# Optimization experiments

Measured on AMD Instinct MI355X. Metric: run time of the kernel, lower is better.

Reference implementation:

```python
import jax, jax.numpy as jnp
import numpy as np

N = 50000      # nodes
H = 128        # hidden_size
RBF = 20       # edge_embedding_size
E_CHE = 400000 # chemical edges
E_VDW = 200000 # van-der-Waals edges


def _prelu(x, a):
    return jnp.where(x > 0, x, a * x)


def _mlp(x, w1, b1, a1, w2, b2, a2):
    # Linear -> PReLU -> Linear -> PReLU (PaiNN message / filter MLP)
    h = _prelu(x @ w1 + b1, a1)
    return _prelu(h @ w2 + b2, a2)


def setup_inputs() -> dict:
    key = jax.random.key(0)
    ks = list(jax.random.split(key, 64))
    it = iter(ks)
    d = {}
    d['node_scalar'] = jax.random.normal(next(it), (N, H), jnp.float32)
    d['node_vector'] = jax.random.normal(next(it), (N, 3, H), jnp.float32)
    for pfx, E in (('che', E_CHE), ('vdw', E_VDW)):
        d[pfx + '_edge'] = jax.random.randint(next(it), (E, 2), 0, N)
        d[pfx + '_edge_diff'] = jax.random.normal(next(it), (E, 3), jnp.float32)
        d[pfx + '_edge_dist'] = jax.random.uniform(next(it), (E,), jnp.float32) + 0.5  # strictly positive
        d[pfx + '_rbf_dist'] = jax.random.normal(next(it), (E, RBF), jnp.float32)
    # four 2-layer MLPs with per-layer PReLU scalar slope (torch default init 0.25)
    def mlp_params(pfx, din):
        s1 = 1.0 / np.sqrt(din)
        s2 = 1.0 / np.sqrt(H)
        d[pfx + '_w1'] = jax.random.uniform(next(it), (din, H), jnp.float32, -s1, s1)
        d[pfx + '_b1'] = jax.random.uniform(next(it), (H,), jnp.float32, -s1, s1)
        d[pfx + '_a1'] = jnp.asarray(0.25, jnp.float32)
        d[pfx + '_w2'] = jax.random.uniform(next(it), (H, 3 * H), jnp.float32, -s2, s2)
        d[pfx + '_b2'] = jax.random.uniform(next(it), (3 * H,), jnp.float32, -s2, s2)
        d[pfx + '_a2'] = jnp.asarray(0.25, jnp.float32)
    mlp_params('che_s', H)    # che scalar message MLP
    mlp_params('che_f', RBF)  # che filter layer
    mlp_params('vdw_s', H)
    mlp_params('vdw_f', RBF)
    return d


def _branch(node_scalar, node_vector, edge, edge_diff, edge_dist, rbf, sp, fp):
    # sp/fp: 6-tuples of MLP params. edge[:,1]=source gather, edge[:,0]=dest scatter.
    scalar_out = _mlp(node_scalar, *sp)          # [N, 3H]
    filter_w = _mlp(rbf, *fp)                    # [E, 3H]
    filter_out = scalar_out[edge[:, 1]] * filter_w  # gather + gate
    gate_vector, message_scalar, gate_edge = jnp.split(filter_out, 3, axis=1)
    state_vector = node_vector[edge[:, 1]] * gate_vector[:, None, :]        # [E,3,H]
    unit = edge_diff / edge_dist[:, None]                                    # [E,3]
    edge_vector = unit[:, :, None] * gate_edge[:, None, :]                   # [E,3,H]
    message_vector = state_vector + edge_vector
    res_scalar = jax.ops.segment_sum(message_scalar, edge[:, 0], num_segments=N)
    res_vector = jax.ops.segment_sum(message_vector, edge[:, 0], num_segments=N)
    return res_scalar, res_vector


def reference(node_scalar, node_vector,
              che_edge, che_edge_diff, che_edge_dist, che_rbf_dist,
              vdw_edge, vdw_edge_diff, vdw_edge_dist, vdw_rbf_dist,
              che_s_w1, che_s_b1, che_s_a1, che_s_w2, che_s_b2, che_s_a2,
              che_f_w1, che_f_b1, che_f_a1, che_f_w2, che_f_b2, che_f_a2,
              vdw_s_w1, vdw_s_b1, vdw_s_a1, vdw_s_w2, vdw_s_b2, vdw_s_a2,
              vdw_f_w1, vdw_f_b1, vdw_f_a1, vdw_f_w2, vdw_f_b2, vdw_f_a2):
    che_sp = (che_s_w1, che_s_b1, che_s_a1, che_s_w2, che_s_b2, che_s_a2)
    che_fp = (che_f_w1, che_f_b1, che_f_a1, che_f_w2, che_f_b2, che_f_a2)
    vdw_sp = (vdw_s_w1, vdw_s_b1, vdw_s_a1, vdw_s_w2, vdw_s_b2, vdw_s_a2)
    vdw_fp = (vdw_f_w1, vdw_f_b1, vdw_f_a1, vdw_f_w2, vdw_f_b2, vdw_f_a2)
    che_rs, che_rv = _branch(node_scalar, node_vector, che_edge, che_edge_diff,
                             che_edge_dist, che_rbf_dist, che_sp, che_fp)
    vdw_rs, vdw_rv = _branch(node_scalar, node_vector, vdw_edge, vdw_edge_diff,
                             vdw_edge_dist, vdw_rbf_dist, vdw_sp, vdw_fp)
    return (node_scalar + che_rs + vdw_rs, node_vector + che_rv + vdw_rv)
```

## Files before the change

### kernel.cpp

```cpp
#include <hip/hip_runtime.h>
#include <hip/hip_bf16.h>

typedef float f32x4 __attribute__((ext_vector_type(4)));
typedef short bf16x8 __attribute__((ext_vector_type(8)));

#define HD 128
#define SCAN_TILE 2048

__device__ __forceinline__ float prelu_f(float x, float a) {
  return x > 0.f ? x : a * x;
}

__device__ __forceinline__ unsigned short f2bf(float x) {
  __hip_bfloat16 h = __float2bfloat16(x);
  return *reinterpret_cast<unsigned short*>(&h);
}
__device__ __forceinline__ float bf2f(unsigned short u) {
  union { unsigned u; float f; } a; a.u = ((unsigned)u) << 16;
  return a.f;
}
__device__ __forceinline__ f32x4 bf4_to_f32(ushort4 u) {
  f32x4 r; r[0] = bf2f(u.x); r[1] = bf2f(u.y); r[2] = bf2f(u.z); r[3] = bf2f(u.w);
  return r;
}

__global__ __launch_bounds__(256) void init_out_kernel(
    const f32x4* __restrict__ ns, const f32x4* __restrict__ nv,
    f32x4* __restrict__ out, int n_ns4, int n_nv4)
{
  int total = n_ns4 + n_nv4;
  for (int i = blockIdx.x * 256 + threadIdx.x; i < total; i += gridDim.x * 256)
    out[i] = (i < n_ns4) ? ns[i] : nv[i - n_ns4];
}

__global__ __launch_bounds__(256) void tconv_kernel(
    const float* __restrict__ src, unsigned short* __restrict__ dst)
{
  int idx = blockIdx.x * 256 + threadIdx.x;
  if (idx < 384 * 128) {
    int c = idx >> 7, k = idx & 127;
    dst[idx] = f2bf(src[(size_t)k * 384 + c]);
  }
}

__global__ __launch_bounds__(256) void tconv_w1e_kernel(
    const float* __restrict__ src, unsigned short* __restrict__ dst)
{
  int idx = blockIdx.x * 256 + threadIdx.x;
  if (idx < 128 * 32) {
    int c = idx >> 5, k = idx & 31;
    dst[idx] = (k < 20) ? f2bf(src[(size_t)k * 128 + c]) : (unsigned short)0;
  }
}

__global__ __launch_bounds__(256) void tconv_w1n_kernel(
    const float* __restrict__ src, unsigned short* __restrict__ dst)
{
  int idx = blockIdx.x * 256 + threadIdx.x;
  if (idx < 128 * 128) {
    int c = idx >> 7, k = idx & 127;
    dst[idx] = f2bf(src[(size_t)k * 128 + c]);
  }
}

__global__ __launch_bounds__(256) void conv_bf16_kernel(
    const f32x4* __restrict__ src, ushort4* __restrict__ dst, int n4)
{
  int i = blockIdx.x * 256 + threadIdx.x;
  if (i < n4) {
    f32x4 v = src[i];
    ushort4 o;
    o.x = f2bf(v[0]); o.y = f2bf(v[1]); o.z = f2bf(v[2]); o.w = f2bf(v[3]);
    dst[i] = o;
  }
}

__global__ __launch_bounds__(256) void node_mlp_mfma(
    const unsigned short* __restrict__ Abf,
    const unsigned short* __restrict__ w1t,
    const float* __restrict__ b1, const float* __restrict__ a1p,
    const unsigned short* __restrict__ w2t,
    const float* __restrict__ b2, const float* __restrict__ a2p,
    unsigned short* __restrict__ out,
    int M)
{
  __shared__ __attribute__((aligned(16))) unsigned short A_lds[64 * HD];
  __shared__ __attribute__((aligned(16))) unsigned short h_lds[64 * HD];
  const int t = threadIdx.x;
  const int wvid = t >> 6, lane = t & 63, l15 = lane & 15, l4 = lane >> 4;
  const int m0 = blockIdx.x * 64;
  const float a1 = a1p[0], a2 = a2p[0];

  for (int idx = t; idx < 64 * HD / 8; idx += 256) {
    int row = idx >> 4, seg = (idx & 15) * 8;
    bf16x8 v = 0;
    if (m0 + row < M) v = *(const bf16x8*)&Abf[(size_t)(m0 + row) * HD + seg];
    *(bf16x8*)&A_lds[row * HD + (seg ^ ((row & 7) << 3))] = v;
  }
  __syncthreads();

  {
    bf16x8 Bf[2][4];
    #pragma unroll
    for (int nf = 0; nf < 2; nf++)
      #pragma unroll
      for (int ks = 0; ks < 4; ks++) {
        int col = wvid * 32 + nf * 16 + l15;
        Bf[nf][ks] = *(const bf16x8*)&w1t[(size_t)col * 128 + ks * 32 + l4 * 8];
      }
    f32x4 D[4][2];
    #pragma unroll
    for (int mi = 0; mi < 4; mi++)
      #pragma unroll
      for (int nf = 0; nf < 2; nf++)
        #pragma unroll
        for (int cc = 0; cc < 4; cc++) D[mi][nf][cc] = 0.f;

    #pragma unroll
    for (int mi = 0; mi < 4; mi++)
      #pragma unroll
      for (int ks = 0; ks < 4; ks++) {
        int row = mi * 16 + l15;
        bf16x8 Af = *(const bf16x8*)&A_lds[row * HD + ((ks * 32 + l4 * 8) ^ ((row & 7) << 3))];
        D[mi][0] = __builtin_amdgcn_mfma_f32_16x16x32_bf16(Af, Bf[0][ks], D[mi][0], 0, 0, 0);
        D[mi][1] = __builtin_amdgcn_mfma_f32_16x16x32_bf16(Af, Bf[1][ks], D[mi][1], 0, 0, 0);
      }

    float b1v0 = b1[wvid * 32 + l15];
    float b1v1 = b1[wvid * 32 + 16 + l15];
    #pragma unroll
    for (int mi = 0; mi < 4; mi++)
      #pragma unroll
      for (int nf = 0; nf < 2; nf++)
        #pragma unroll
        for (int r4 = 0; r4 < 4; r4++) {
          int row = mi * 16 + l4 * 4 + r4;
          int col = wvid * 32 + nf * 16 + l15;
          h_lds[row * HD + (col ^ ((row & 7) << 3))] =
              f2bf(prelu_f(D[mi][nf][r4] + (nf ? b1v1 : b1v0), a1));
        }
  }
  __syncthreads();

  for (int m = 0; m < 3; m++) {
    bf16x8 Bf[2][4];
    #pragma unroll
    for (int nf = 0; nf < 2; nf++)
      #pragma unroll
      for (int ks = 0; ks < 4; ks++) {
        int col = m * 128 + wvid * 32 + nf * 16 + l15;
        Bf[nf][ks] = *(const bf16x8*)&w2t[(size_t)col * 128 + ks * 32 + l4 * 8];
      }
    f32x4 D[4][2];
    #pragma unroll
    for (int mi = 0; mi < 4; mi++)
      #pragma unroll
      for (int nf = 0; nf < 2; nf++)
        #pragma unroll
        for (int cc = 0; cc < 4; cc++) D[mi][nf][cc] = 0.f;

    #pragma unroll
    for (int mi = 0; mi < 4; mi++)
      #pragma unroll
      for (int ks = 0; ks < 4; ks++) {
        int row = mi * 16 + l15;
        bf16x8 Af = *(const bf16x8*)&h_lds[row * HD + ((ks * 32 + l4 * 8) ^ ((row & 7) << 3))];
        D[mi][0] = __builtin_amdgcn_mfma_f32_16x16x32_bf16(Af, Bf[0][ks], D[mi][0], 0, 0, 0);
        D[mi][1] = __builtin_amdgcn_mfma_f32_16x16x32_bf16(Af, Bf[1][ks], D[mi][1], 0, 0, 0);
      }

    float b2v0 = b2[m * 128 + wvid * 32 + l15];
    float b2v1 = b2[m * 128 + wvid * 32 + 16 + l15];
    #pragma unroll
    for (int mi = 0; mi < 4; mi++)
      #pragma unroll
      for (int nf = 0; nf < 2; nf++)
        #pragma unroll
        for (int r4 = 0; r4 < 4; r4++) {
          int row = mi * 16 + l4 * 4 + r4;
          if (m0 + row < M) {
            int col = m * 128 + wvid * 32 + nf * 16 + l15;
            out[(size_t)(m0 + row) * 384 + col] =
                f2bf(prelu_f(D[mi][nf][r4] + (nf ? b2v1 : b2v0), a2));
          }
        }
  }
}

__global__ __launch_bounds__(256) void zero_int_kernel(int* __restrict__ p, int n) {
  int i = blockIdx.x * 256 + threadIdx.x;
  if (i < n) p[i] = 0;
}

__global__ __launch_bounds__(256) void hist_kernel(const int* __restrict__ edge, int* __restrict__ counts, int E) {
  int e = blockIdx.x * 256 + threadIdx.x;
  if (e < E) atomicAdd(&counts[edge[(size_t)e * 2]], 1);
}

__global__ __launch_bounds__(256) void scan_partial_kernel(
    const int* __restrict__ counts, int* __restrict__ partials, int n)
{
  const int b = blockIdx.x, t = threadIdx.x;
  const int base = b * SCAN_TILE + t * 8;
  int s = 0;
  #pragma unroll
  for (int i = 0; i < 8; i++) {
    int idx = base + i;
    if (idx < n) s += counts[idx];
  }
  __shared__ int sums[256];
  sums[t] = s;
  __syncthreads();
  for (int o = 128; o > 0; o >>= 1) {
    if (t < o) sums[t] += sums[t + o];
    __syncthreads();
  }
  if (t == 0) partials[b] = sums[0];
}

__global__ __launch_bounds__(256) void scan_partials_kernel(int* __restrict__ partials, int nb)
{
  __shared__ int s[256];
  const int t = threadIdx.x;
  s[t] = (t < nb) ? partials[t] : 0;
  __syncthreads();
  for (int o = 1; o < 256; o <<= 1) {
    int v = s[t];
    int u = (t >= o) ? s[t - o] : 0;
    __syncthreads();
    s[t] = v + u;
    __syncthreads();
  }
  if (t < nb) partials[t] = (t == 0) ? 0 : s[t - 1];
}

__global__ __launch_bounds__(256) void scan_write_kernel(
    const int* __restrict__ counts, const int* __restrict__ partials,
    int* __restrict__ offsets, int* __restrict__ cursor, int n, int E)
{
  const int b = blockIdx.x, t = threadIdx.x;
  const int base = b * SCAN_TILE + t * 8;
  int vals[8];
  int s = 0;
  #pragma unroll
  for (int i = 0; i < 8; i++) {
    int idx = base + i;
    vals[i] = (idx < n) ? counts[idx] : 0;
    s += vals[i];
  }
  __shared__ int sums[256];
  sums[t] = s;
  __syncthreads();
  for (int o = 1; o < 256; o <<= 1) {
    int v = sums[t];
    int u = (t >= o) ? sums[t - o] : 0;
    __syncthreads();
    sums[t] = v + u;
    __syncthreads();
  }
  int run = partials[b] + ((t == 0) ? 0 : sums[t - 1]);
  #pragma unroll
  for (int i = 0; i < 8; i++) {
    int idx = base + i;
    if (idx < n) {
      offsets[idx] = run;
      cursor[idx] = run;
      run += vals[i];
    }
  }
  if (b == 0 && t == 0) offsets[n] = E;
}

__global__ __launch_bounds__(256) void scatter_ids_kernel(
    const int* __restrict__ edge, int* __restrict__ cursor, int* __restrict__ edge_list, int E)
{
  int e = blockIdx.x * 256 + threadIdx.x;
  if (e < E) {
    int d = edge[(size_t)e * 2];
    int p = atomicAdd(&cursor[d], 1);
    edge_list[p] = e;
  }
}

__global__ __launch_bounds__(256) void permute_edge_kernel(
    const int* __restrict__ edge_list,
    const int* __restrict__ edge, const float* __restrict__ diff,
    const float* __restrict__ dist, const float* __restrict__ rbf,
    int* __restrict__ src_s, int* __restrict__ dst_s,
    float4* __restrict__ unit_s, unsigned short* __restrict__ rbf_b,
    int E)
{
  int p = blockIdx.x * 256 + threadIdx.x;
  if (p >= E) return;
  int e = edge_list[p];
  src_s[p] = edge[(size_t)e * 2 + 1];
  dst_s[p] = edge[(size_t)e * 2 + 0];
  float inv = 1.f / dist[e];
  float4 u;
  u.x = diff[(size_t)e * 3 + 0] * inv;
  u.y = diff[(size_t)e * 3 + 1] * inv;
  u.z = diff[(size_t)e * 3 + 2] * inv;
  u.w = 0.f;
  unit_s[p] = u;
  ushort4* ro = (ushort4*)(rbf_b + (size_t)p * 32);
  const float* rr = &rbf[(size_t)e * 20];
  #pragma unroll
  for (int i = 0; i < 5; i++) {
    ushort4 o;
    o.x = f2bf(rr[4 * i + 0]); o.y = f2bf(rr[4 * i + 1]);
    o.z = f2bf(rr[4 * i + 2]); o.w = f2bf(rr[4 * i + 3]);
    ro[i] = o;
  }
  ushort4 z; z.x = 0; z.y = 0; z.z = 0; z.w = 0;
  ro[5] = z; ro[6] = z; ro[7] = z;
}

__global__ __launch_bounds__(256) void edge_mfma_reduce_kernel(
    const unsigned short* __restrict__ so,
    const unsigned short* __restrict__ nv,
    const int*   __restrict__ src_s,
    const int*   __restrict__ dst_s,
    const float4* __restrict__ unit_s,
    const unsigned short* __restrict__ rbf_b,
    const int*   __restrict__ offsets,
    const unsigned short* __restrict__ w1t,
    const float* __restrict__ b1, const float* __restrict__ a1p,
    const unsigned short* __restrict__ w2t,
    const float* __restrict__ b2, const float* __restrict__ a2p,
    float* __restrict__ out,
    int N, int E)
{
  __shared__ __attribute__((aligned(16))) unsigned short A1_lds[64 * 40];
  __shared__ __attribute__((aligned(16))) unsigned short h_lds[64 * HD];
  __shared__ __attribute__((aligned(16))) unsigned short P_lds[3][64 * HD];
  __shared__ int src_l[64];
  __shared__ float unit_l[64][3];
  __shared__ int run_rs[65], run_node[64], run_flag[64];
  __shared__ int nd_s;

  const int t = threadIdx.x;
  const int tx = t & 31, ty = t >> 5;
  const int c4 = tx * 4;
  const int wvid = t >> 6, lane = t & 63, l15 = lane & 15, l4 = lane >> 4;
  const int pblk = blockIdx.x * 64;
  const int nrows = min(64, E - pblk);
  const float a1 = a1p[0], a2 = a2p[0];

  if (t < 64) {
    int d = -1, s = 0;
    float ux = 0.f, uy = 0.f, uz = 0.f;
    if (t < nrows) {
      s = src_s[pblk + t];
      d = dst_s[pblk + t];
      float4 u = unit_s[pblk + t];
      ux = u.x; uy = u.y; uz = u.z;
    }
    src_l[t] = s;
    unit_l[t][0] = ux; unit_l[t][1] = uy; unit_l[t][2] = uz;
    int dprev = __shfl_up(d, 1);
    bool flag = (t < nrows) && (t == 0 || d != dprev);
    unsigned long long mask = __ballot(flag ? 1 : 0);
    if (flag) {
      int j = __popcll(mask & ((1ull << t) - 1ull));
      run_rs[j] = t;
      run_node[j] = d;
      unsigned long long rest = (t == 63) ? 0ull : (mask >> (t + 1));
      int re = rest ? (t + 1 + (__ffsll((long long)rest) - 1)) : nrows;
      int interior = 1;
      if (t == 0 && offsets[d] != pblk) interior = 0;
      if (re == nrows && offsets[d + 1] != pblk + nrows) interior = 0;
      run_flag[j] = interior;
    }
    if (t == 0) {
      int nd = __popcll(mask);
      nd_s = nd;
      run_rs[nd] = nrows;
    }
  }

  {
    const bf16x8* rb = (const bf16x8*)(rbf_b + (size_t)pblk * 32);
    int row = t >> 2, seg = (t & 3) * 8;
    *(bf16x8*)&A1_lds[row * 40 + seg] = rb[t];
  }
  __syncthreads();

  {
    bf16x8 B1[2];
    B1[0] = *(const bf16x8*)&w1t[(size_t)(wvid * 32 + l15) * 32 + l4 * 8];
    B1[1] = *(const bf16x8*)&w1t[(size_t)(wvid * 32 + 16 + l15) * 32 + l4 * 8];
    f32x4 D1[4][2];
    #pragma unroll
    for (int mi = 0; mi < 4; mi++)
      #pragma unroll
      for (int nf = 0; nf < 2; nf++)
        #pragma unroll
        for (int cc = 0; cc < 4; cc++) D1[mi][nf][cc] = 0.f;

    #pragma unroll
    for (int mi = 0; mi < 4; mi++) {
      bf16x8 Af = *(const bf16x8*)&A1_lds[(mi * 16 + l15) * 40 + l4 * 8];
      D1[mi][0] = __builtin_amdgcn_mfma_f32_16x16x32_bf16(Af, B1[0], D1[mi][0], 0, 0, 0);
      D1[mi][1] = __builtin_amdgcn_mfma_f32_16x16x32_bf16(Af, B1[1], D1[mi][1], 0, 0, 0);
    }

    float b1v0 = b1[wvid * 32 + l15];
    float b1v1 = b1[wvid * 32 + 16 + l15];
    #pragma unroll
    for (int mi = 0; mi < 4; mi++)
      #pragma unroll
      for (int nf = 0; nf < 2; nf++)
        #pragma unroll
        for (int r4 = 0; r4 < 4; r4++) {
          int row = mi * 16 + l4 * 4 + r4;
          int col = wvid * 32 + nf * 16 + l15;
          h_lds[row * HD + (col ^ ((row & 7) << 3))] =
              f2bf(prelu_f(D1[mi][nf][r4] + (nf ? b1v1 : b1v0), a1));
        }
  }
  __syncthreads();

  for (int m = 0; m < 3; m++) {
    bf16x8 Bf[2][4];
    #pragma unroll
    for (int nf = 0; nf < 2; nf++)
      #pragma unroll
      for (int ks = 0; ks < 4; ks++) {
        int col = m * 128 + wvid * 32 + nf * 16 + l15;
        Bf[nf][ks] = *(const bf16x8*)&w2t[(size_t)col * 128 + ks * 32 + l4 * 8];
      }
    f32x4 D[4][2];
    #pragma unroll
    for (int mi = 0; mi < 4; mi++)
      #pragma unroll
      for (int nf = 0; nf < 2; nf++)
        #pragma unroll
        for (int cc = 0; cc < 4; cc++) D[mi][nf][cc] = 0.f;

    #pragma unroll
    for (int mi = 0; mi < 4; mi++)
      #pragma unroll
      for (int ks = 0; ks < 4; ks++) {
        int row = mi * 16 + l15;
        bf16x8 Af = *(const bf16x8*)&h_lds[row * HD + ((ks * 32 + l4 * 8) ^ ((row & 7) << 3))];
        D[mi][0] = __builtin_amdgcn_mfma_f32_16x16x32_bf16(Af, Bf[0][ks], D[mi][0], 0, 0, 0);
        D[mi][1] = __builtin_amdgcn_mfma_f32_16x16x32_bf16(Af, Bf[1][ks], D[mi][1], 0, 0, 0);
      }

    float b2v0 = b2[m * 128 + wvid * 32 + l15];
    float b2v1 = b2[m * 128 + wvid * 32 + 16 + l15];
    #pragma unroll
    for (int mi = 0; mi < 4; mi++)
      #pragma unroll
      for (int nf = 0; nf < 2; nf++)
        #pragma unroll
        for (int r4 = 0; r4 < 4; r4++) {
          int row = mi * 16 + l4 * 4 + r4;
          int col = wvid * 32 + nf * 16 + l15;
          float v = prelu_f(D[mi][nf][r4] + (nf ? b2v1 : b2v0), a2);
          P_lds[m][row * HD + (col ^ ((row & 7) << 3))] = f2bf(v);
        }
  }
  __syncthreads();

  #pragma unroll
  for (int rr = 0; rr < 8; rr++) {
    const int r = ty * 8 + rr;
    const int src = src_l[r];
    const int sc = c4 ^ ((r & 7) << 3);
    f32x4 gvp = bf4_to_f32(*(const ushort4*)&P_lds[0][r * HD + sc]);
    f32x4 msp = bf4_to_f32(*(const ushort4*)&P_lds[1][r * HD + sc]);
    f32x4 gep = bf4_to_f32(*(const ushort4*)&P_lds[2][r * HD + sc]);
    const size_t sb = (size_t)src * 384;
    f32x4 s0 = bf4_to_f32(*(const ushort4*)&so[sb + c4]);
    f32x4 s1 = bf4_to_f32(*(const ushort4*)&so[sb + HD + c4]);
    f32x4 s2 = bf4_to_f32(*(const ushort4*)&so[sb + 2 * HD + c4]);
    f32x4 v0 = bf4_to_f32(*(const ushort4*)&nv[sb + c4]);
    f32x4 v1 = bf4_to_f32(*(const ushort4*)&nv[sb + HD + c4]);
    f32x4 v2 = bf4_to_f32(*(const ushort4*)&nv[sb + 2 * HD + c4]);
    const float u0 = unit_l[r][0], u1 = unit_l[r][1], u2 = unit_l[r][2];
    ushort4 msw, m0w, m1w, m2w;
    #pragma unroll
    for (int cc = 0; cc < 4; cc++) {
      float gv = gvp[cc] * s0[cc];
      float ms = msp[cc] * s1[cc];
      float ge = gep[cc] * s2[cc];
      float mv0 = v0[cc] * gv + u0 * ge;
      float mv1 = v1[cc] * gv + u1 * ge;
      float mv2 = v2[cc] * gv + u2 * ge;
      ((unsigned short*)&msw)[cc] = f2bf(ms);
      ((unsigned short*)&m0w)[cc] = f2bf(mv0);
      ((unsigned short*)&m1w)[cc] = f2bf(mv1);
      ((unsigned short*)&m2w)[cc] = f2bf(mv2);
    }
    *(ushort4*)&h_lds[r * HD + sc]    = msw;
    *(ushort4*)&P_lds[0][r * HD + sc] = m0w;
    *(ushort4*)&P_lds[1][r * HD + sc] = m1w;
    *(ushort4*)&P_lds[2][r * HD + sc] = m2w;
  }
  __syncthreads();

  {
    const int pl = t >> 6;
    const int c2 = (t & 63) * 2;
    const unsigned short* region = (pl == 0) ? h_lds : &P_lds[pl - 1][0];
    float* out_v = out + (size_t)N * HD;
    const int nd = nd_s;
    for (int j = 0; j < nd; j++) {
      const int rs = run_rs[j], re = run_rs[j + 1];
      const int n = run_node[j];
      float a0 = 0.f, a1v = 0.f;
      for (int r = rs; r < re; r++) {
        int ad = r * HD + (((c2 & ~3) ^ ((r & 7) << 3)) | (c2 & 3));
        unsigned int u = *(const unsigned int*)&region[ad];
        a0  += bf2f((unsigned short)(u & 0xffffu));
        a1v += bf2f((unsigned short)(u >> 16));
      }
      float* dstp = (pl == 0) ? (out + (size_t)n * HD + c2)
                              : (out_v + (size_t)n * 384 + (size_t)(pl - 1) * HD + c2);
      if (run_flag[j]) {
        float2 cur = *(float2*)dstp;
        cur.x += a0; cur.y += a1v;
        *(float2*)dstp = cur;
      } else {
        atomicAdd(dstp, a0);
        atomicAdd(dstp + 1, a1v);
      }
    }
  }
}

extern "C" void kernel_launch(void* const* d_in, const int* in_sizes, int n_in,
                              void* d_out, int out_size, void* d_ws, size_t ws_size,
                              hipStream_t stream)
{
  const float* node_scalar = (const float*)d_in[0];
  const float* node_vector = (const float*)d_in[1];
  const int*   che_edge = (const int*)d_in[2];
  const float* che_diff = (const float*)d_in[3];
  const float* che_dist = (const float*)d_in[4];
  const float* che_rbf  = (const float*)d_in[5];
  const int*   vdw_edge = (const int*)d_in[6];
  const float* vdw_diff = (const float*)d_in[7];
  const float* vdw_dist = (const float*)d_in[8];
  const float* vdw_rbf  = (const float*)d_in[9];
  const float* mlp_p[24];
  for (int i = 0; i < 24; i++) mlp_p[i] = (const float*)d_in[10 + i];

  const int N = in_sizes[0] / HD;
  const int E_che = in_sizes[4];
  const int E_vdw = in_sizes[8];
  const int E_max = E_che > E_vdw ? E_che : E_vdw;
  const int E_pad = (E_max + 63) & ~63;
  const int nb_scan = (N + SCAN_TILE - 1) / SCAN_TILE;

  char* wp = (char*)d_ws;
  size_t off = 0;
  unsigned short* so_bf = (unsigned short*)(wp + off); off += (size_t)N * 384 * 2;
  unsigned short* nv_bf = (unsigned short*)(wp + off); off += (size_t)N * 384 * 2;
  unsigned short* ns_bf = (unsigned short*)(wp + off); off += (size_t)N * 128 * 2;
  int* counts     = (int*)(wp + off);   off += (size_t)N * 4;
  int* cursor     = (int*)(wp + off);   off += (size_t)N * 4;
  int* offsets    = (int*)(wp + off);   off += (size_t)(N + 1) * 4;
  int* partials   = (int*)(wp + off);   off += 256 * 4;
  off = (off + 255) & ~(size_t)255;
  int* edge_list  = (int*)(wp + off);   off += (size_t)E_max * 4;
  int* src_s      = (int*)(wp + off);   off += (size_t)E_max * 4;
  int* dst_s      = (int*)(wp + off);   off += (size_t)E_max * 4;
  off = (off + 255) & ~(size_t)255;
  float4* unit_s  = (float4*)(wp + off); off += (size_t)E_max * 16;
  unsigned short* rbf_b = (unsigned short*)(wp + off); off += (size_t)E_pad * 64;
  off = (off + 255) & ~(size_t)255;
  unsigned short* w2t_sche = (unsigned short*)(wp + off); off += 384 * 128 * 2;
  unsigned short* w2t_fche = (unsigned short*)(wp + off); off += 384 * 128 * 2;
  unsigned short* w2t_svdw = (unsigned short*)(wp + off); off += 384 * 128 * 2;
  unsigned short* w2t_fvdw = (unsigned short*)(wp + off); off += 384 * 128 * 2;
  unsigned short* w1t_nche = (unsigned short*)(wp + off); off += 128 * 128 * 2;
  unsigned short* w1t_nvdw = (unsigned short*)(wp + off); off += 128 * 128 * 2;
  unsigned short* w1t_eche = (unsigned short*)(wp + off); off += 128 * 32 * 2;
  unsigned short* w1t_evdw = (unsigned short*)(wp + off); off += 128 * 32 * 2;

  const int n_ns4 = N * HD / 4;
  const int n_nv4 = N * 3 * HD / 4;
  init_out_kernel<<<2048, 256, 0, stream>>>(
      (const f32x4*)node_scalar, (const f32x4*)node_vector, (f32x4*)d_out, n_ns4, n_nv4);

  conv_bf16_kernel<<<(n_nv4 + 255) / 256, 256, 0, stream>>>(
      (const f32x4*)node_vector, (ushort4*)nv_bf, n_nv4);
  conv_bf16_kernel<<<(n_ns4 + 255) / 256, 256, 0, stream>>>(
      (const f32x4*)node_scalar, (ushort4*)ns_bf, n_ns4);

  tconv_kernel<<<192, 256, 0, stream>>>(mlp_p[3],  w2t_sche);
  tconv_kernel<<<192, 256, 0, stream>>>(mlp_p[9],  w2t_fche);
  tconv_kernel<<<192, 256, 0, stream>>>(mlp_p[15], w2t_svdw);
  tconv_kernel<<<192, 256, 0, stream>>>(mlp_p[21], w2t_fvdw);
  tconv_w1n_kernel<<<64, 256, 0, stream>>>(mlp_p[0],  w1t_nche);
  tconv_w1n_kernel<<<64, 256, 0, stream>>>(mlp_p[12], w1t_nvdw);
  tconv_w1e_kernel<<<16, 256, 0, stream>>>(mlp_p[6],  w1t_eche);
  tconv_w1e_kernel<<<16, 256, 0, stream>>>(mlp_p[18], w1t_evdw);

  for (int br = 0; br < 2; br++) {
    const int*   edge = br == 0 ? che_edge : vdw_edge;
    const float* diff = br == 0 ? che_diff : vdw_diff;
    const float* dist = br == 0 ? che_dist : vdw_dist;
    const float* rbf  = br == 0 ? che_rbf  : vdw_rbf;
    const int    E    = br == 0 ? E_che : E_vdw;
    const float* const* sp = &mlp_p[br == 0 ? 0 : 12];
    const float* const* fp = &mlp_p[br == 0 ? 6 : 18];
    const unsigned short* w2t_s = br == 0 ? w2t_sche : w2t_svdw;
    const unsigned short* w2t_f = br == 0 ? w2t_fche : w2t_fvdw;
    const unsigned short* w1t_n = br == 0 ? w1t_nche : w1t_nvdw;
    const unsigned short* w1t_e = br == 0 ? w1t_eche : w1t_evdw;

    node_mlp_mfma<<<(N + 63) / 64, 256, 0, stream>>>(
        ns_bf, w1t_n, sp[1], sp[2], w2t_s, sp[4], sp[5], so_bf, N);

    zero_int_kernel<<<(N + 255) / 256, 256, 0, stream>>>(counts, N);
    hist_kernel<<<(E + 255) / 256, 256, 0, stream>>>(edge, counts, E);
    scan_partial_kernel<<<nb_scan, 256, 0, stream>>>(counts, partials, N);
    scan_partials_kernel<<<1, 256, 0, stream>>>(partials, nb_scan);
    scan_write_kernel<<<nb_scan, 256, 0, stream>>>(counts, partials, offsets, cursor, N, E);
    scatter_ids_kernel<<<(E + 255) / 256, 256, 0, stream>>>(edge, cursor, edge_list, E);
    permute_edge_kernel<<<(E + 255) / 256, 256, 0, stream>>>(
        edge_list, edge, diff, dist, rbf, src_s, dst_s, unit_s, rbf_b, E);

    edge_mfma_reduce_kernel<<<(E + 63) / 64, 256, 0, stream>>>(
        so_bf, nv_bf, src_s, dst_s, unit_s, rbf_b, offsets,
        w1t_e, fp[1], fp[2], w2t_f, fp[4], fp[5],
        (float*)d_out, N, E);
  }
}
```

Baseline: 753.1 us.

## Halve edge tile to 32 rows for occupancy and fuse init with bf16 conversion

The edge MFMA/reduce kernel now processes 32 edges per block instead of 64. This roughly halves its LDS footprint, and it adds a launch-bounds hint of 4 blocks per CU so more blocks can be resident and latency is better hidden. In exchange, each block reloads the filter weights for half as many edges, and the number of blocks and run-boundary atomics doubles. Separately, the output initialisation and the two fp32-to-bf16 node conversions are merged into one kernel, so the node inputs are read once and two launches are saved.

```diff
diff --git a/kernel.cpp b/kernel.cpp
--- a/kernel.cpp
+++ b/kernel.cpp
@@ -5,6 +5,7 @@
 typedef short bf16x8 __attribute__((ext_vector_type(8)));
 
 #define HD 128
+#define TILE 32
 #define SCAN_TILE 2048
 
 __device__ __forceinline__ float prelu_f(float x, float a) {
@@ -24,13 +25,19 @@
   return r;
 }
 
-__global__ __launch_bounds__(256) void init_out_kernel(
+__global__ __launch_bounds__(256) void init_conv_kernel(
     const f32x4* __restrict__ ns, const f32x4* __restrict__ nv,
-    f32x4* __restrict__ out, int n_ns4, int n_nv4)
+    f32x4* __restrict__ out, ushort4* __restrict__ ns_bf, ushort4* __restrict__ nv_bf,
+    int n_ns4, int n_nv4)
 {
   int total = n_ns4 + n_nv4;
-  for (int i = blockIdx.x * 256 + threadIdx.x; i < total; i += gridDim.x * 256)
-    out[i] = (i < n_ns4) ? ns[i] : nv[i - n_ns4];
+  for (int i = blockIdx.x * 256 + threadIdx.x; i < total; i += gridDim.x * 256) {
+    f32x4 v = (i < n_ns4) ? ns[i] : nv[i - n_ns4];
+    out[i] = v;
+    ushort4 o;
+    o.x = f2bf(v[0]); o.y = f2bf(v[1]); o.z = f2bf(v[2]); o.w = f2bf(v[3]);
+    if (i < n_ns4) ns_bf[i] = o; else nv_bf[i - n_ns4] = o;
+  }
 }
 
 __global__ __launch_bounds__(256) void tconv_kernel(
@@ -60,18 +67,6 @@
   if (idx < 128 * 128) {
     int c = idx >> 7, k = idx & 127;
     dst[idx] = f2bf(src[(size_t)k * 128 + c]);
-  }
-}
-
-__global__ __launch_bounds__(256) void conv_bf16_kernel(
-    const f32x4* __restrict__ src, ushort4* __restrict__ dst, int n4)
-{
-  int i = blockIdx.x * 256 + threadIdx.x;
-  if (i < n4) {
-    f32x4 v = src[i];
-    ushort4 o;
-    o.x = f2bf(v[0]); o.y = f2bf(v[1]); o.z = f2bf(v[2]); o.w = f2bf(v[3]);
-    dst[i] = o;
   }
 }
 
@@ -315,7 +310,7 @@
   ro[5] = z; ro[6] = z; ro[7] = z;
 }
 
-__global__ __launch_bounds__(256) void edge_mfma_reduce_kernel(
+__global__ __launch_bounds__(256, 4) void edge_mfma_reduce_kernel(
     const unsigned short* __restrict__ so,
     const unsigned short* __restrict__ nv,
     const int*   __restrict__ src_s,
@@ -330,20 +325,20 @@
     float* __restrict__ out,
     int N, int E)
 {
-  __shared__ __attribute__((aligned(16))) unsigned short A1_lds[64 * 40];
-  __shared__ __attribute__((aligned(16))) unsigned short h_lds[64 * HD];
-  __shared__ __attribute__((aligned(16))) unsigned short P_lds[3][64 * HD];
-  __shared__ int src_l[64];
-  __shared__ float unit_l[64][3];
-  __shared__ int run_rs[65], run_node[64], run_flag[64];
+  __shared__ __attribute__((aligned(16))) unsigned short A1_lds[TILE * 40];
+  __shared__ __attribute__((aligned(16))) unsigned short h_lds[TILE * HD];
+  __shared__ __attribute__((aligned(16))) unsigned short P_lds[3][TILE * HD];
+  __shared__ int src_l[TILE];
+  __shared__ float unit_l[TILE][3];
+  __shared__ int run_rs[TILE + 1], run_node[TILE], run_flag[TILE];
   __shared__ int nd_s;
 
   const int t = threadIdx.x;
   const int tx = t & 31, ty = t >> 5;
   const int c4 = tx * 4;
   const int wvid = t >> 6, lane = t & 63, l15 = lane & 15, l4 = lane >> 4;
-  const int pblk = blockIdx.x * 64;
-  const int nrows = min(64, E - pblk);
+  const int pblk = blockIdx.x * TILE;
+  const int nrows = min(TILE, E - pblk);
   const float a1 = a1p[0], a2 = a2p[0];
 
   if (t < 64) {
@@ -355,8 +350,10 @@
       float4 u = unit_s[pblk + t];
       ux = u.x; uy = u.y; uz = u.z;
     }
-    src_l[t] = s;
-    unit_l[t][0] = ux; unit_l[t][1] = uy; unit_l[t][2] = uz;
+    if (t < TILE) {
+      src_l[t] = s;
+      unit_l[t][0] = ux; unit_l[t][1] = uy; unit_l[t][2] = uz;
+    }
     int dprev = __shfl_up(d, 1);
     bool flag = (t < nrows) && (t == 0 || d != dprev);
     unsigned long long mask = __ballot(flag ? 1 : 0);
@@ -378,7 +375,7 @@
     }
   }
 
-  {
+  if (t < TILE * 4) {
     const bf16x8* rb = (const bf16x8*)(rbf_b + (size_t)pblk * 32);
     int row = t >> 2, seg = (t & 3) * 8;
     *(bf16x8*)&A1_lds[row * 40 + seg] = rb[t];
@@ -389,16 +386,16 @@
     bf16x8 B1[2];
     B1[0] = *(const bf16x8*)&w1t[(size_t)(wvid * 32 + l15) * 32 + l4 * 8];
     B1[1] = *(const bf16x8*)&w1t[(size_t)(wvid * 32 + 16 + l15) * 32 + l4 * 8];
-    f32x4 D1[4][2];
-    #pragma unroll
-    for (int mi = 0; mi < 4; mi++)
+    f32x4 D1[2][2];
+    #pragma unroll
+    for (int mi = 0; mi < 2; mi++)
       #pragma unroll
       for (int nf = 0; nf < 2; nf++)
         #pragma unroll
         for (int cc = 0; cc < 4; cc++) D1[mi][nf][cc] = 0.f;
 
     #pragma unroll
-    for (int mi = 0; mi < 4; mi++) {
+    for (int mi = 0; mi < 2; mi++) {
       bf16x8 Af = *(const bf16x8*)&A1_lds[(mi * 16 + l15) * 40 + l4 * 8];
       D1[mi][0] = __builtin_amdgcn_mfma_f32_16x16x32_bf16(Af, B1[0], D1[mi][0], 0, 0, 0);
       D1[mi][1] = __builtin_amdgcn_mfma_f32_16x16x32_bf16(Af, B1[1], D1[mi][1], 0, 0, 0);
@@ -407,7 +404,7 @@
     float b1v0 = b1[wvid * 32 + l15];
     float b1v1 = b1[wvid * 32 + 16 + l15];
     #pragma unroll
-    for (int mi = 0; mi < 4; mi++)
+    for (int mi = 0; mi < 2; mi++)
       #pragma unroll
       for (int nf = 0; nf < 2; nf++)
         #pragma unroll
@@ -429,16 +426,16 @@
         int col = m * 128 + wvid * 32 + nf * 16 + l15;
         Bf[nf][ks] = *(const bf16x8*)&w2t[(size_t)col * 128 + ks * 32 + l4 * 8];
       }
-    f32x4 D[4][2];
-    #pragma unroll
-    for (int mi = 0; mi < 4; mi++)
+    f32x4 D[2][2];
+    #pragma unroll
+    for (int mi = 0; mi < 2; mi++)
       #pragma unroll
       for (int nf = 0; nf < 2; nf++)
         #pragma unroll
         for (int cc = 0; cc < 4; cc++) D[mi][nf][cc] = 0.f;
 
     #pragma unroll
-    for (int mi = 0; mi < 4; mi++)
+    for (int mi = 0; mi < 2; mi++)
       #pragma unroll
       for (int ks = 0; ks < 4; ks++) {
         int row = mi * 16 + l15;
@@ -450,7 +447,7 @@
     float b2v0 = b2[m * 128 + wvid * 32 + l15];
     float b2v1 = b2[m * 128 + wvid * 32 + 16 + l15];
     #pragma unroll
-    for (int mi = 0; mi < 4; mi++)
+    for (int mi = 0; mi < 2; mi++)
       #pragma unroll
       for (int nf = 0; nf < 2; nf++)
         #pragma unroll
@@ -464,8 +461,8 @@
   __syncthreads();
 
   #pragma unroll
-  for (int rr = 0; rr < 8; rr++) {
-    const int r = ty * 8 + rr;
+  for (int rr = 0; rr < 4; rr++) {
+    const int r = ty * 4 + rr;
     const int src = src_l[r];
     const int sc = c4 ^ ((r & 7) << 3);
     f32x4 gvp = bf4_to_f32(*(const ushort4*)&P_lds[0][r * HD + sc]);
@@ -582,13 +579,9 @@
 
   const int n_ns4 = N * HD / 4;
   const int n_nv4 = N * 3 * HD / 4;
-  init_out_kernel<<<2048, 256, 0, stream>>>(
-      (const f32x4*)node_scalar, (const f32x4*)node_vector, (f32x4*)d_out, n_ns4, n_nv4);
-
-  conv_bf16_kernel<<<(n_nv4 + 255) / 256, 256, 0, stream>>>(
-      (const f32x4*)node_vector, (ushort4*)nv_bf, n_nv4);
-  conv_bf16_kernel<<<(n_ns4 + 255) / 256, 256, 0, stream>>>(
-      (const f32x4*)node_scalar, (ushort4*)ns_bf, n_ns4);
+  init_conv_kernel<<<2048, 256, 0, stream>>>(
+      (const f32x4*)node_scalar, (const f32x4*)node_vector, (f32x4*)d_out,
+      (ushort4*)ns_bf, (ushort4*)nv_bf, n_ns4, n_nv4);
 
   tconv_kernel<<<192, 256, 0, stream>>>(mlp_p[3],  w2t_sche);
   tconv_kernel<<<192, 256, 0, stream>>>(mlp_p[9],  w2t_fche);
@@ -624,7 +617,7 @@
     permute_edge_kernel<<<(E + 255) / 256, 256, 0, stream>>>(
         edge_list, edge, diff, dist, rbf, src_s, dst_s, unit_s, rbf_b, E);
 
-    edge_mfma_reduce_kernel<<<(E + 63) / 64, 256, 0, stream>>>(
+    edge_mfma_reduce_kernel<<<(E + TILE - 1) / TILE, 256, 0, stream>>>(
         so_bf, nv_bf, src_s, dst_s, unit_s, rbf_b, offsets,
         w1t_e, fp[1], fp[2], w2t_f, fp[4], fp[5],
         (float*)d_out, N, E);
```

After: 650.2 us. 1.16x faster.
